# Optimization experiments

Hardware: AMD Instinct MI355X
Metric: run time of the kernel (lower is better)

Reference implementation:

```python
import jax, jax.numpy as jnp
import numpy as np
from functools import partial

ENC = 128  # encoding_dim

def setup_inputs() -> dict:
    key = jax.random.key(0)
    ks = jax.random.split(key, 6)
    B, S, E, H = 8, 512, 128, 512
    action_sequence = jax.random.normal(ks[0], (B, S, E), dtype=jnp.float32)
    # nn.Linear-style init scale ~ 1/sqrt(fan_in)
    W1 = jax.random.normal(ks[1], (H, E), dtype=jnp.float32) / np.sqrt(E)
    b1 = jnp.zeros((H,), dtype=jnp.float32)
    W2 = jax.random.normal(ks[2], (ENC * ENC, H), dtype=jnp.float32) / np.sqrt(H)
    b2 = jnp.zeros((ENC * ENC,), dtype=jnp.float32)
    e0 = jax.random.normal(ks[3], (1, ENC), dtype=jnp.float32) / 10.0
    return {"action_sequence": action_sequence, "W1": W1, "b1": b1,
            "W2": W2, "b2": b2, "e0": e0}

def reference(action_sequence, W1, b1, W2, b2, e0):
    B, S, E = action_sequence.shape
    # fast-weight generation: two dense layers
    hidden = jnp.tanh(jnp.einsum('bse,he->bsh', action_sequence, W1) + b1)
    Wa = (jnp.einsum('bsh,oh->bso', hidden, W2) + b2).reshape(B, S, ENC, ENC)
    # attractor dynamics: et_{i} = clamp(et_{i-1} @ Wa[:, i], -5, 5)
    e0b = jnp.broadcast_to(e0, (B, ENC))
    Wa_seq = jnp.transpose(Wa[:, 1:], (1, 0, 2, 3))  # [S-1, B, ENC, ENC]
    def step(et, Wa_i):
        et_next = jnp.clip(jnp.einsum('bd,bde->be', et, Wa_i), -5.0, 5.0)
        return et_next, et_next
    _, es = jax.lax.scan(step, e0b, Wa_seq)  # [S-1, B, ENC]
    encodings = jnp.concatenate([e0b[None], es], axis=0)  # [S, B, ENC]
    return jnp.transpose(encodings, (1, 0, 2))  # [B, S, ENC]
```

## Files before the change

kernel.cpp:

```cpp
#include <hip/hip_runtime.h>
#include <cstddef>

#define BB 8
#define SS 512
#define EE 128
#define HH 512
#define ENC 128

__device__ __forceinline__ float xla_tanhf(float x) {
    const float cx = fminf(fmaxf(x, -9.0f), 9.0f);
    const float x2 = __fmul_rn(cx, cx);
    float p = -2.76076847742355e-16f;
    p = __fadd_rn(__fmul_rn(p, x2), 2.00018790482477e-13f);
    p = __fadd_rn(__fmul_rn(p, x2), -8.60467152213735e-11f);
    p = __fadd_rn(__fmul_rn(p, x2), 5.12229709037114e-08f);
    p = __fadd_rn(__fmul_rn(p, x2), 1.48572235717979e-05f);
    p = __fadd_rn(__fmul_rn(p, x2), 6.37261928875436e-04f);
    p = __fadd_rn(__fmul_rn(p, x2), 4.89352455891786e-03f);
    const float num = __fmul_rn(cx, p);
    float q = 1.19825839466702e-06f;
    q = __fadd_rn(__fmul_rn(q, x2), 1.18534705686654e-04f);
    q = __fadd_rn(__fmul_rn(q, x2), 2.26843463243900e-03f);
    q = __fadd_rn(__fmul_rn(q, x2), 4.89352518554385e-03f);
    const float r = __fdiv_rn(num, q);
    return (fabsf(x) < 0.0004f) ? x : r;
}

__device__ __forceinline__ int arow_map(int m, int chm1, int chsh, int i0) {
    return ((m >> chsh) * SS) + i0 + (m & chm1);
}

template <int ACT, int MAPROW, int TRANSP>
__global__ __launch_bounds__(256) void gemm_nt(const float* __restrict__ A,
                                               const float* __restrict__ Bm,
                                               const float* __restrict__ bias,
                                               float* __restrict__ C,
                                               int N, int K,
                                               int chm1, int chsh, int i0) {
    __shared__ float As[16][128];
    __shared__ float Bs[16][128];

    const int tid = threadIdx.x;
    const int tx = tid & 15;
    const int ty = tid >> 4;
    const int n0 = blockIdx.x * 128;
    const int m0 = blockIdx.y * 128;
    const int bd = blockIdx.x >> 4;
    const int be = blockIdx.x & 15;

    const int lr = tid >> 2;
    const int lc = (tid & 3) << 2;

    const int ga0 = MAPROW ? arow_map(m0 + lr, chm1, chsh, i0) : (m0 + lr);
    const int ga1 = MAPROW ? arow_map(m0 + lr + 64, chm1, chsh, i0) : (m0 + lr + 64);

    const int r0 = lr, r1 = lr + 64;
    const int gb0 = TRANSP ? ((bd * 16 + (r0 >> 3)) * 128 + be * 8 + (r0 & 7))
                           : (n0 + r0);
    const int gb1 = TRANSP ? ((bd * 16 + (r1 >> 3)) * 128 + be * 8 + (r1 & 7))
                           : (n0 + r1);

    float acc[8][8];
#pragma unroll
    for (int i = 0; i < 8; ++i)
#pragma unroll
        for (int j = 0; j < 8; ++j) acc[i][j] = 0.f;

    for (int k0 = 0; k0 < K; k0 += 16) {
        const float4 a0 = *(const float4*)(A + (size_t)ga0 * K + (k0 + lc));
        const float4 a1 = *(const float4*)(A + (size_t)ga1 * K + (k0 + lc));
        const float4 b0 = *(const float4*)(Bm + (size_t)gb0 * K + (k0 + lc));
        const float4 b1 = *(const float4*)(Bm + (size_t)gb1 * K + (k0 + lc));

        __syncthreads();

        As[lc + 0][lr] = a0.x; As[lc + 1][lr] = a0.y;
        As[lc + 2][lr] = a0.z; As[lc + 3][lr] = a0.w;
        As[lc + 0][lr + 64] = a1.x; As[lc + 1][lr + 64] = a1.y;
        As[lc + 2][lr + 64] = a1.z; As[lc + 3][lr + 64] = a1.w;
        Bs[lc + 0][lr] = b0.x; Bs[lc + 1][lr] = b0.y;
        Bs[lc + 2][lr] = b0.z; Bs[lc + 3][lr] = b0.w;
        Bs[lc + 0][lr + 64] = b1.x; Bs[lc + 1][lr + 64] = b1.y;
        Bs[lc + 2][lr + 64] = b1.z; Bs[lc + 3][lr + 64] = b1.w;

        __syncthreads();

#pragma unroll
        for (int k = 0; k < 16; ++k) {
            const float4 av0 = *(const float4*)&As[k][ty * 8];
            const float4 av1 = *(const float4*)&As[k][ty * 8 + 4];
            const float4 bv0 = *(const float4*)&Bs[k][tx * 8];
            const float4 bv1 = *(const float4*)&Bs[k][tx * 8 + 4];
            const float a[8] = {av0.x, av0.y, av0.z, av0.w, av1.x, av1.y, av1.z, av1.w};
            const float b[8] = {bv0.x, bv0.y, bv0.z, bv0.w, bv1.x, bv1.y, bv1.z, bv1.w};
#pragma unroll
            for (int i = 0; i < 8; ++i)
#pragma unroll
                for (int j = 0; j < 8; ++j)
                    acc[i][j] = __fadd_rn(acc[i][j], __fmul_rn(a[i], b[j]));
        }
    }

#pragma unroll
    for (int i = 0; i < 8; ++i) {
        const int m = m0 + ty * 8 + i;
        if (TRANSP) {
            const int d = bd * 16 + tx;
#pragma unroll
            for (int j = 0; j < 8; ++j) {
                const int ee = be * 8 + j;
                const int o = d * 128 + ee;
                const float v = __fadd_rn(acc[i][j], bias[o]);
                C[(size_t)m * N + ((size_t)(d >> 2) * 128 + ee) * 4 + (d & 3)] = v;
            }
        } else {
            float v[8];
#pragma unroll
            for (int j = 0; j < 8; ++j) {
                const int n = n0 + tx * 8 + j;
                v[j] = __fadd_rn(acc[i][j], bias[n]);
                if (ACT) v[j] = xla_tanhf(v[j]);
            }
            float4* dst = (float4*)(C + (size_t)m * N + (n0 + tx * 8));
            dst[0] = make_float4(v[0], v[1], v[2], v[3]);
            dst[1] = make_float4(v[4], v[5], v[6], v[7]);
        }
    }
}

__device__ __forceinline__ void scan_barrier_nodrain() {
    asm volatile("s_waitcnt lgkmcnt(0)" ::: "memory");
    __builtin_amdgcn_s_barrier();
    asm volatile("" ::: "memory");
}

#define SCAN_CONSUME(Q, BUF)                                                \
    {                                                                       \
              \
        _Pragma("unroll")                                                   \
        for (int dq = 0; dq < 8; ++dq) {                                    \
            const float4 t4 = *(const float4*)&et[s][(Q) * 32 + dq * 4];    \
            const float4 wv = BUF[dq];       \
            sum = __fadd_rn(sum, __fmul_rn(t4.x, wv.x));                    \
            sum = __fadd_rn(sum, __fmul_rn(t4.y, wv.y));                    \
            sum = __fadd_rn(sum, __fmul_rn(t4.z, wv.z));                    \
            sum = __fadd_rn(sum, __fmul_rn(t4.w, wv.w));                    \
        }                                                                   \
    }

#define SCAN_REFILL(BUF)                                                    \
    {                                                                       \
         \
        _Pragma("unroll")                                                   \
        for (int u = 0; u < 8; ++u) BUF[u] = Pf[u * 128];                   \
        Pf += 1024;                                                         \
        asm volatile("" ::: "memory");                                      \
    }

#define SCAN_STEP(B0, B1, B2, B3)                                           \
    {                                                                       \
        float sum = 0.f;  \
        SCAN_CONSUME(0, B0) SCAN_REFILL(B0)                                 \
        SCAN_CONSUME(1, B1) SCAN_REFILL(B1)                                 \
        SCAN_CONSUME(2, B2) SCAN_REFILL(B2)                                 \
        SCAN_CONSUME(3, B3) SCAN_REFILL(B3)                                 \
        const float v = fminf(fmaxf(sum, -5.f), 5.f);         \
        out[((size_t)b * SS + (i0 + ii)) * ENC + e] = v;                    \
        et[s ^ 1][e] = v;                                                   \
        scan_barrier_nodrain();   \
        s ^= 1;                                                             \
        ++ii;                                                               \
    }

__global__ __launch_bounds__(128, 1) void scan_kernel(const float* __restrict__ Wa,
                                                      const float* __restrict__ e0,
                                                      float* __restrict__ et_state,
                                                      float* __restrict__ out,
                                                      int i0, int CH) {
    __shared__ float et[2][128];
    const int b = blockIdx.x;
    const int e = threadIdx.x;

    int s = 0;
    if (i0 == 0) {
        const float v = e0[e];
        et[0][e] = v;
        out[(size_t)b * SS * ENC + e] = v;
    } else {
        et[0][e] = et_state[b * 128 + e];
    }
    __syncthreads();

    const int start = (i0 == 0) ? 1 : 0;
    const float4* Wb4 = (const float4*)(Wa + (size_t)b * CH * (ENC * ENC));

    float4 w0[8], w1[8], w2[8], w3[8], w4[8], w5[8], w6[8], w7[8];
    const float4* Pq = Wb4 + (size_t)start * 4096 + e;
#pragma unroll
    for (int u = 0; u < 8; ++u) w0[u] = Pq[u * 128];
#pragma unroll
    for (int u = 0; u < 8; ++u) w1[u] = Pq[(8 + u) * 128];
#pragma unroll
    for (int u = 0; u < 8; ++u) w2[u] = Pq[(16 + u) * 128];
#pragma unroll
    for (int u = 0; u < 8; ++u) w3[u] = Pq[(24 + u) * 128];
#pragma unroll
    for (int u = 0; u < 8; ++u) w4[u] = Pq[(32 + u) * 128];
#pragma unroll
    for (int u = 0; u < 8; ++u) w5[u] = Pq[(40 + u) * 128];
#pragma unroll
    for (int u = 0; u < 8; ++u) w6[u] = Pq[(48 + u) * 128];
#pragma unroll
    for (int u = 0; u < 8; ++u) w7[u] = Pq[(56 + u) * 128];
    const float4* Pf = Pq + 8192;
    asm volatile("" ::: "memory");

    int ii = start;
    const int pairs = (CH - start) >> 1;
    const int odd = (CH - start) & 1;

    for (int p = 0; p < pairs; ++p) {
        SCAN_STEP(w0, w1, w2, w3)
        SCAN_STEP(w4, w5, w6, w7)
    }
    if (odd) {
        float sum = 0.f;
        SCAN_CONSUME(0, w0)
        SCAN_CONSUME(1, w1)
        SCAN_CONSUME(2, w2)
        SCAN_CONSUME(3, w3)
        const float v = fminf(fmaxf(sum, -5.f), 5.f);
        out[((size_t)b * SS + (i0 + ii)) * ENC + e] = v;
        et[s ^ 1][e] = v;
        scan_barrier_nodrain();
        s ^= 1;
    }
    et_state[b * 128 + e] = et[s][e];
}

extern "C" void kernel_launch(void* const* d_in, const int* in_sizes, int n_in,
                              void* d_out, int out_size, void* d_ws, size_t ws_size,
                              hipStream_t stream) {
    const float* A  = (const float*)d_in[0];
    const float* W1 = (const float*)d_in[1];
    const float* b1 = (const float*)d_in[2];
    const float* W2 = (const float*)d_in[3];
    const float* b2 = (const float*)d_in[4];
    const float* e0 = (const float*)d_in[5];
    float* out = (float*)d_out;

    const size_t WA_PAD = 163840;
    int CH = 16;
    for (int c = 512; c >= 16; c >>= 1) {
        const size_t Mc = (size_t)BB * c;
        const size_t need = 4096 + Mc * HH * sizeof(float) +
                            Mc * (size_t)(ENC * ENC) * sizeof(float) + WA_PAD;
        if (need <= ws_size) { CH = c; break; }
    }
    const int Mc = BB * CH;
    int chsh = 0;
    while ((1 << chsh) < CH) ++chsh;
    const int chm1 = CH - 1;

    float* et_state = (float*)d_ws;
    float* hidden   = (float*)((char*)d_ws + 4096);
    float* Wa       = hidden + (size_t)Mc * HH;

    for (int i0 = 0; i0 < SS; i0 += CH) {
        dim3 g1(HH / 128, Mc / 128);
        gemm_nt<1, 1, 0><<<g1, 256, 0, stream>>>(A, W1, b1, hidden, HH, EE,
                                                 chm1, chsh, i0);
        dim3 g2((ENC * ENC) / 128, Mc / 128);
        gemm_nt<0, 0, 1><<<g2, 256, 0, stream>>>(hidden, W2, b2, Wa, ENC * ENC,
                                                 HH, 0, 0, 0);
        scan_kernel<<<BB, 128, 0, stream>>>(Wa, e0, et_state, out, i0, CH);
    }
}
```

Baseline: 1.560 ms.

## Pad GEMM shared tiles, split B-fragment columns, and shrink scan prefetch ring

```diff
diff --git a/kernel.cpp b/kernel.cpp
--- a/kernel.cpp
+++ b/kernel.cpp
@@ -37,8 +37,8 @@
                                                float* __restrict__ C,
                                                int N, int K,
                                                int chm1, int chsh, int i0) {
-    __shared__ float As[16][128];
-    __shared__ float Bs[16][128];
+    __shared__ float As[16][132];
+    __shared__ float Bs[16][132];
 
     const int tid = threadIdx.x;
     const int tx = tid & 15;
@@ -89,8 +89,8 @@
         for (int k = 0; k < 16; ++k) {
             const float4 av0 = *(const float4*)&As[k][ty * 8];
             const float4 av1 = *(const float4*)&As[k][ty * 8 + 4];
-            const float4 bv0 = *(const float4*)&Bs[k][tx * 8];
-            const float4 bv1 = *(const float4*)&Bs[k][tx * 8 + 4];
+            const float4 bv0 = *(const float4*)&Bs[k][tx * 4];
+            const float4 bv1 = *(const float4*)&Bs[k][64 + tx * 4];
             const float a[8] = {av0.x, av0.y, av0.z, av0.w, av1.x, av1.y, av1.z, av1.w};
             const float b[8] = {bv0.x, bv0.y, bv0.z, bv0.w, bv1.x, bv1.y, bv1.z, bv1.w};
 #pragma unroll
@@ -105,10 +105,11 @@
     for (int i = 0; i < 8; ++i) {
         const int m = m0 + ty * 8 + i;
         if (TRANSP) {
-            const int d = bd * 16 + tx;
 #pragma unroll
             for (int j = 0; j < 8; ++j) {
-                const int ee = be * 8 + j;
+                const int c = (j < 4) ? (tx * 4 + j) : (64 + tx * 4 + (j - 4));
+                const int d = bd * 16 + (c >> 3);
+                const int ee = be * 8 + (c & 7);
                 const int o = d * 128 + ee;
                 const float v = __fadd_rn(acc[i][j], bias[o]);
                 C[(size_t)m * N + ((size_t)(d >> 2) * 128 + ee) * 4 + (d & 3)] = v;
@@ -116,14 +117,21 @@
         } else {
             float v[8];
 #pragma unroll
-            for (int j = 0; j < 8; ++j) {
-                const int n = n0 + tx * 8 + j;
+            for (int j = 0; j < 4; ++j) {
+                const int n = n0 + tx * 4 + j;
                 v[j] = __fadd_rn(acc[i][j], bias[n]);
                 if (ACT) v[j] = xla_tanhf(v[j]);
             }
-            float4* dst = (float4*)(C + (size_t)m * N + (n0 + tx * 8));
-            dst[0] = make_float4(v[0], v[1], v[2], v[3]);
-            dst[1] = make_float4(v[4], v[5], v[6], v[7]);
+#pragma unroll
+            for (int j = 4; j < 8; ++j) {
+                const int n = n0 + 64 + tx * 4 + (j - 4);
+                v[j] = __fadd_rn(acc[i][j], bias[n]);
+                if (ACT) v[j] = xla_tanhf(v[j]);
+            }
+            *(float4*)(C + (size_t)m * N + (n0 + tx * 4)) =
+                make_float4(v[0], v[1], v[2], v[3]);
+            *(float4*)(C + (size_t)m * N + (n0 + 64 + tx * 4)) =
+                make_float4(v[4], v[5], v[6], v[7]);
         }
     }
 }
@@ -134,42 +142,26 @@
     asm volatile("" ::: "memory");
 }
 
-#define SCAN_CONSUME(Q, BUF)                                                \
+#define SCAN_QUARTER(Q, WC, WP)                                             \
     {                                                                       \
+                                                             \
+        const int pf = (ii - start) * 4 + (Q) + 3;                          \
+        const int pfc = (pf < nq) ? pf : (nq - 1);      \
+        const float4* P4 = Wb4 + (size_t)(start + (pfc >> 2)) * 4096        \
+                               + (size_t)(pfc & 3) * 1024 + e;              \
+        _Pragma("unroll")                                                   \
+        for (int u = 0; u < 8; ++u) WP[u] = P4[u * 128];                    \
+        asm volatile("" ::: "memory");                                      \
               \
         _Pragma("unroll")                                                   \
         for (int dq = 0; dq < 8; ++dq) {                                    \
             const float4 t4 = *(const float4*)&et[s][(Q) * 32 + dq * 4];    \
-            const float4 wv = BUF[dq];       \
+            const float4 wv = WC[dq];        \
             sum = __fadd_rn(sum, __fmul_rn(t4.x, wv.x));                    \
             sum = __fadd_rn(sum, __fmul_rn(t4.y, wv.y));                    \
             sum = __fadd_rn(sum, __fmul_rn(t4.z, wv.z));                    \
             sum = __fadd_rn(sum, __fmul_rn(t4.w, wv.w));                    \
         }                                                                   \
-    }
-
-#define SCAN_REFILL(BUF)                                                    \
-    {                                                                       \
-         \
-        _Pragma("unroll")                                                   \
-        for (int u = 0; u < 8; ++u) BUF[u] = Pf[u * 128];                   \
-        Pf += 1024;                                                         \
-        asm volatile("" ::: "memory");                                      \
-    }
-
-#define SCAN_STEP(B0, B1, B2, B3)                                           \
-    {                                                                       \
-        float sum = 0.f;  \
-        SCAN_CONSUME(0, B0) SCAN_REFILL(B0)                                 \
-        SCAN_CONSUME(1, B1) SCAN_REFILL(B1)                                 \
-        SCAN_CONSUME(2, B2) SCAN_REFILL(B2)                                 \
-        SCAN_CONSUME(3, B3) SCAN_REFILL(B3)                                 \
-        const float v = fminf(fmaxf(sum, -5.f), 5.f);         \
-        out[((size_t)b * SS + (i0 + ii)) * ENC + e] = v;                    \
-        et[s ^ 1][e] = v;                                                   \
-        scan_barrier_nodrain();   \
-        s ^= 1;                                                             \
-        ++ii;                                                               \
     }
 
 __global__ __launch_bounds__(128, 1) void scan_kernel(const float* __restrict__ Wa,
@@ -193,42 +185,27 @@
 
     const int start = (i0 == 0) ? 1 : 0;
     const float4* Wb4 = (const float4*)(Wa + (size_t)b * CH * (ENC * ENC));
-
-    float4 w0[8], w1[8], w2[8], w3[8], w4[8], w5[8], w6[8], w7[8];
-    const float4* Pq = Wb4 + (size_t)start * 4096 + e;
-#pragma unroll
-    for (int u = 0; u < 8; ++u) w0[u] = Pq[u * 128];
-#pragma unroll
-    for (int u = 0; u < 8; ++u) w1[u] = Pq[(8 + u) * 128];
-#pragma unroll
-    for (int u = 0; u < 8; ++u) w2[u] = Pq[(16 + u) * 128];
-#pragma unroll
-    for (int u = 0; u < 8; ++u) w3[u] = Pq[(24 + u) * 128];
-#pragma unroll
-    for (int u = 0; u < 8; ++u) w4[u] = Pq[(32 + u) * 128];
-#pragma unroll
-    for (int u = 0; u < 8; ++u) w5[u] = Pq[(40 + u) * 128];
-#pragma unroll
-    for (int u = 0; u < 8; ++u) w6[u] = Pq[(48 + u) * 128];
-#pragma unroll
-    for (int u = 0; u < 8; ++u) w7[u] = Pq[(56 + u) * 128];
-    const float4* Pf = Pq + 8192;
+    const int nq = (CH - start) * 4;
+
+    float4 w0[8], w1[8], w2[8], w3[8];
+
+    {
+        const float4* S4 = Wb4 + (size_t)start * 4096 + e;
+#pragma unroll
+        for (int u = 0; u < 8; ++u) w0[u] = S4[u * 128];
+#pragma unroll
+        for (int u = 0; u < 8; ++u) w1[u] = S4[(8 + u) * 128];
+#pragma unroll
+        for (int u = 0; u < 8; ++u) w2[u] = S4[(16 + u) * 128];
+    }
     asm volatile("" ::: "memory");
 
-    int ii = start;
-    const int pairs = (CH - start) >> 1;
-    const int odd = (CH - start) & 1;
-
-    for (int p = 0; p < pairs; ++p) {
-        SCAN_STEP(w0, w1, w2, w3)
-        SCAN_STEP(w4, w5, w6, w7)
-    }
-    if (odd) {
+    for (int ii = start; ii < CH; ++ii) {
         float sum = 0.f;
-        SCAN_CONSUME(0, w0)
-        SCAN_CONSUME(1, w1)
-        SCAN_CONSUME(2, w2)
-        SCAN_CONSUME(3, w3)
+        SCAN_QUARTER(0, w0, w3)
+        SCAN_QUARTER(1, w1, w0)
+        SCAN_QUARTER(2, w2, w1)
+        SCAN_QUARTER(3, w3, w2)
         const float v = fminf(fmaxf(sum, -5.f), 5.f);
         out[((size_t)b * SS + (i0 + ii)) * ENC + e] = v;
         et[s ^ 1][e] = v;
@@ -249,12 +226,11 @@
     const float* e0 = (const float*)d_in[5];
     float* out = (float*)d_out;
 
-    const size_t WA_PAD = 163840;
     int CH = 16;
     for (int c = 512; c >= 16; c >>= 1) {
         const size_t Mc = (size_t)BB * c;
         const size_t need = 4096 + Mc * HH * sizeof(float) +
-                            Mc * (size_t)(ENC * ENC) * sizeof(float) + WA_PAD;
+                            Mc * (size_t)(ENC * ENC) * sizeof(float);
         if (need <= ws_size) { CH = c; break; }
     }
     const int Mc = BB * CH;
```

New measurement: 1.394 ms. 1.12x faster.
